# Optimization experiments

Hardware: AMD Instinct MI355X
Metric: run time of the kernel (lower is better)

The kernel has to match this reference:

```python
import jax, jax.numpy as jnp
import numpy as np

N = 50000      # nodes
E = 800000     # edges (avg degree 16)
H = 128        # hidden_channels
F = 128        # num_filters
G = 50         # num_gaussians
L = 6          # num_interactions
CUT = 10.0     # cutoff
H2 = H // 2
OUT = 12


def ssp(x):
    # ShiftedSoftplus: softplus(x) - log(2)
    return jax.nn.softplus(x) - jnp.log(2.0)


def setup_inputs() -> dict:
    key = jax.random.key(0)
    ks = jax.random.split(key, 16)
    s = 0.05
    x_atoms = jax.random.randint(ks[0], (N,), 0, 100)
    edge_index = jax.random.randint(ks[1], (2, E), 0, N)
    edge_attr = jax.random.uniform(ks[2], (E,), minval=0.05, maxval=CUT)
    return {
        "x_atoms": x_atoms,
        "edge_index": edge_index,
        "edge_attr": edge_attr,
        "embedding": jax.random.normal(ks[3], (100, H)) * s,
        # per-interaction stacked params [L, ...]
        "mlp_w1": jax.random.normal(ks[4], (L, G, F)) * s,
        "mlp_b1": jnp.zeros((L, F)),
        "mlp_w2": jax.random.normal(ks[5], (L, F, F)) * s,
        "mlp_b2": jnp.zeros((L, F)),
        "conv1_w": jax.random.normal(ks[6], (L, H, F)) * s,   # CFConv.lin1 (no bias)
        "conv2_w": jax.random.normal(ks[7], (L, F, H)) * s,   # CFConv.lin2
        "conv2_b": jnp.zeros((L, H)),
        "int_lin_w": jax.random.normal(ks[8], (L, H, H)) * s,  # InteractionBlock.lin
        "int_lin_b": jnp.zeros((L, H)),
        # head
        "lin1_w": jax.random.normal(ks[9], (H, H2)) * s,
        "lin1_b": jnp.zeros((H2,)),
        "lin2_w": jax.random.normal(ks[10], (H2, H2)) * s,
        "lin2_b": jnp.zeros((H2,)),
        "readout_w": jax.random.normal(ks[11], (H2, OUT)) * s,
        "readout_b": jnp.zeros((OUT,)),
    }


def reference(x_atoms, edge_index, edge_attr, embedding,
              mlp_w1, mlp_b1, mlp_w2, mlp_b2,
              conv1_w, conv2_w, conv2_b, int_lin_w, int_lin_b,
              lin1_w, lin1_b, lin2_w, lin2_b, readout_w, readout_b):
    h = embedding[x_atoms]  # [N, H]

    # Gaussian smearing of distances -> [E, G]
    offset = jnp.linspace(0.0, CUT, G)
    coeff = -0.5 / (offset[1] - offset[0]) ** 2
    ed = jnp.exp(coeff * (edge_attr[:, None] - offset) ** 2)

    # cosine cutoff weight per edge
    C = 0.5 * (jnp.cos(edge_attr * jnp.pi / CUT) + 1.0)  # [E]

    src = edge_index[0]
    dst = edge_index[1]

    for l in range(L):
        # filter network on expanded distances -> [E, F]
        W = ssp(ed @ mlp_w1[l] + mlp_b1[l]) @ mlp_w2[l] + mlp_b2[l]
        W = W * C[:, None]
        xf = h @ conv1_w[l]                     # [N, F]
        msg = xf[src] * W                        # gather + modulate, [E, F]
        agg = jax.ops.segment_sum(msg, dst, num_segments=N)  # scatter-add, [N, F]
        v = agg @ conv2_w[l] + conv2_b[l]        # [N, H]
        v = ssp(v)
        v = v @ int_lin_w[l] + int_lin_b[l]
        h = h + v                                # residual

    h = ssp(h @ lin1_w + lin1_b)
    h = h @ lin2_w + lin2_b
    h_agg = jnp.sum(h, axis=0, keepdims=True)    # [1, H2]
    return h_agg @ readout_w + readout_b         # [1, OUT]
```

## Files before the change

### kernel.cpp

```cpp
#include <hip/hip_runtime.h>
#include <hip/hip_bf16.h>
#include <math.h>

#define NN 50000
#define EE 800000
#define HH 128
#define FF 128
#define GG 50
#define LL 6
#define H2D 64
#define OUT_DIM 12
#define NK 4096
#define NBLK 782
#define SB 196

typedef __bf16 bf16;
typedef __attribute__((ext_vector_type(8))) __bf16 bf16x8;
typedef __attribute__((ext_vector_type(4))) __bf16 bf16x4;
typedef __attribute__((ext_vector_type(4))) float f32x4;
typedef __attribute__((ext_vector_type(4))) unsigned u32x4;

#define DEV __device__ __forceinline__

DEV float sspf(float x) {
    return fmaxf(x, 0.f) + __logf(1.f + __expf(-fabsf(x))) - 0.69314718055994531f;
}

DEV f32x4 mfma16(bf16x8 a, bf16x8 b, f32x4 c) {
    return __builtin_amdgcn_mfma_f32_16x16x32_bf16(a, b, c, 0, 0, 0);
}

DEV float blo(unsigned u) { return __uint_as_float(u << 16); }
DEV float bhi(unsigned u) { return __uint_as_float(u & 0xffff0000u); }

struct PrepArgs {
    const float *conv1_w, *conv2_w, *int_lin_w, *mlp_w1, *mlp_w2, *lin1_w, *lin2_w;
    bf16 *c1t, *c2t, *ilt, *w1t, *w2t, *l1t, *l2t;
};

__global__ void prep_kernel(PrepArgs p) {
    int j = blockIdx.x;
    const float* src = nullptr; bf16* dst = nullptr; int R = 0, C = 0, K = 0;
    if (j < 30) {
        int l = j / 5, m = j % 5;
        switch (m) {
            case 0: src = p.conv1_w + l * HH * FF;   dst = p.c1t + l * FF * HH;  R = HH; C = FF; K = HH; break;
            case 1: src = p.conv2_w + l * FF * HH;   dst = p.c2t + l * HH * FF;  R = FF; C = HH; K = FF; break;
            case 2: src = p.int_lin_w + l * HH * HH; dst = p.ilt + l * HH * HH;  R = HH; C = HH; K = HH; break;
            case 3: src = p.mlp_w1 + l * GG * FF;    dst = p.w1t + l * FF * 64;  R = GG; C = FF; K = 64; break;
            case 4: src = p.mlp_w2 + l * FF * FF;    dst = p.w2t + l * FF * FF;  R = FF; C = FF; K = FF; break;
        }
    } else if (j == 30) { src = p.lin1_w; dst = p.l1t; R = HH;  C = H2D; K = HH; }
    else                { src = p.lin2_w; dst = p.l2t; R = H2D; C = H2D; K = H2D; }
    int total = C * K;
    for (int idx = threadIdx.x; idx < total; idx += blockDim.x) {
        int c = idx / K, r = idx - c * K;
        dst[idx] = (r < R) ? (bf16)src[r * C + c] : (bf16)0.f;
    }
}

__global__ __launch_bounds__(256) void table_kernel(const bf16* __restrict__ w1t,
                                                    const bf16* __restrict__ w2t,
                                                    const float* __restrict__ mlp_b1,
                                                    const float* __restrict__ mlp_b2,
                                                    bf16* __restrict__ tab) {
    __shared__ bf16 sW1[128 * 72];
    __shared__ bf16 sW2[128 * 136];
    __shared__ bf16 sT1[64 * 136];
    int tid = threadIdx.x;
    int l = blockIdx.x / 65, rb = blockIdx.x % 65;
    const bf16* W1 = w1t + (size_t)l * 128 * 64;
    const bf16* W2 = w2t + (size_t)l * 128 * 128;
    for (int idx = tid * 8; idx < 128 * 64; idx += 2048) {
        int n = idx >> 6, k = idx & 63;
        *(bf16x8*)&sW1[n * 72 + k] = *(const bf16x8*)(W1 + idx);
    }
    for (int idx = tid * 8; idx < 128 * 128; idx += 2048) {
        int n = idx >> 7, k = idx & 127;
        *(bf16x8*)&sW2[n * 136 + k] = *(const bf16x8*)(W2 + idx);
    }
    int w = tid >> 6, lane = tid & 63, ln = lane & 15, kg = lane >> 4;
    int rowt = rb * 64 + w * 16;
    float d1 = (float)min(rowt + ln, NK) * (10.f / NK);
    const float step = 10.f / 49.f;
    const float coeff = -0.5f / (step * step);
    __syncthreads();
    f32x4 acc[8] = {};
#pragma unroll
    for (int k0 = 0; k0 < 64; k0 += 32) {
        bf16x8 a;
#pragma unroll
        for (int jj = 0; jj < 8; jj++) {
            int g = k0 + kg * 8 + jj;
            float diff = d1 - g * step;
            float v = (g < GG) ? __expf(coeff * diff * diff) : 0.f;
            a[jj] = (bf16)v;
        }
#pragma unroll
        for (int t = 0; t < 8; t++) {
            bf16x8 b = *(const bf16x8*)&sW1[(t * 16 + ln) * 72 + k0 + kg * 8];
            acc[t] = mfma16(a, b, acc[t]);
        }
    }
    const float* b1 = mlp_b1 + l * FF;
#pragma unroll
    for (int t = 0; t < 8; t++) {
        int colt = t * 16 + ln;
        float bb = b1[colt];
#pragma unroll
        for (int r = 0; r < 4; r++)
            sT1[(w * 16 + kg * 4 + r) * 136 + colt] = (bf16)sspf(acc[t][r] + bb);
    }
    __syncthreads();
    f32x4 acc2[8] = {};
#pragma unroll
    for (int k0 = 0; k0 < 128; k0 += 32) {
        bf16x8 a = *(const bf16x8*)&sT1[(w * 16 + ln) * 136 + k0 + kg * 8];
#pragma unroll
        for (int t = 0; t < 8; t++) {
            bf16x8 b = *(const bf16x8*)&sW2[(t * 16 + ln) * 136 + k0 + kg * 8];
            acc2[t] = mfma16(a, b, acc2[t]);
        }
    }
    const float* b2 = mlp_b2 + l * FF;
    float Cw[4]; int rrow[4];
#pragma unroll
    for (int r = 0; r < 4; r++) {
        int rr = rowt + kg * 4 + r;
        rrow[r] = rr;
        float dd = (float)min(rr, NK) * (10.f / NK);
        Cw[r] = 0.5f * (cosf(dd * 0.31415926535897932f) + 1.f);
    }
#pragma unroll
    for (int t = 0; t < 8; t++) {
        int colt = t * 16 + ln;
        float bb = b2[colt];
#pragma unroll
        for (int r = 0; r < 4; r++) {
            if (rrow[r] <= NK)
                tab[((size_t)l * (NK + 1) + rrow[r]) * FF + colt] = (bf16)((acc2[t][r] + bb) * Cw[r]);
        }
    }
}

__global__ void hist_kernel(const int* __restrict__ eidx, int* __restrict__ hist) {
    int e = blockIdx.x * 256 + threadIdx.x;
    if (e < EE) atomicAdd(&hist[eidx[EE + e]], 1);
}

__global__ __launch_bounds__(256) void scanA_kernel(const int* __restrict__ hist,
                                                    int* __restrict__ bsum) {
    __shared__ int red[256];
    int t = threadIdx.x;
    int i = blockIdx.x * 256 + t;
    int v = (i < NN) ? hist[i] : 0;
    red[t] = v;
    __syncthreads();
    for (int off = 128; off > 0; off >>= 1) {
        if (t < off) red[t] += red[t + off];
        __syncthreads();
    }
    if (t == 0) bsum[blockIdx.x] = red[0];
}

__global__ __launch_bounds__(256) void scanB_kernel(int* __restrict__ bsum) {
    __shared__ int buf[256];
    int t = threadIdx.x;
    int v = (t < SB) ? bsum[t] : 0;
    buf[t] = v;
    __syncthreads();
    for (int off = 1; off < 256; off <<= 1) {
        int y = (t >= off) ? buf[t - off] : 0;
        __syncthreads();
        buf[t] += y;
        __syncthreads();
    }
    if (t < SB) bsum[t] = buf[t] - v;
}

__global__ __launch_bounds__(256) void scanC_kernel(const int* __restrict__ hist,
                                                    const int* __restrict__ bsum,
                                                    int* __restrict__ rs,
                                                    int* __restrict__ cur) {
    __shared__ int buf[256];
    int t = threadIdx.x;
    int i = blockIdx.x * 256 + t;
    int v = (i < NN) ? hist[i] : 0;
    buf[t] = v;
    __syncthreads();
    for (int off = 1; off < 256; off <<= 1) {
        int y = (t >= off) ? buf[t - off] : 0;
        __syncthreads();
        buf[t] += y;
        __syncthreads();
    }
    if (i < NN) {
        int ex = buf[t] - v + bsum[blockIdx.x];
        rs[i] = ex;
        cur[i] = ex;
    }
}

__global__ void scatter_kernel(const float* __restrict__ eattr, const int* __restrict__ eidx,
                               int* __restrict__ cur, int* __restrict__ es) {
    int e = blockIdx.x * 256 + threadIdx.x;
    if (e < EE) {
        int dd = eidx[EE + e];
        int pos = atomicAdd(&cur[dd], 1);
        int k = (int)(eattr[e] * ((float)NK / 10.f) + 0.5f);
        k = min(k, NK);
        es[pos] = k | (eidx[e] << 13);
    }
}

__global__ void embed_kernel(const int* __restrict__ x_atoms, const float* __restrict__ emb,
                             bf16* __restrict__ hb) {
    int idx = blockIdx.x * blockDim.x + threadIdx.x;
    if (idx >= NN * 16) return;
    int n = idx >> 4, ch = idx & 15;
    int a = x_atoms[n];
    const float* ep = emb + a * HH + ch * 8;
    f32x4 v0 = *(const f32x4*)ep;
    f32x4 v1 = *(const f32x4*)(ep + 4);
    bf16x8 vb;
#pragma unroll
    for (int q = 0; q < 4; q++) { vb[q] = (bf16)v0[q]; vb[q + 4] = (bf16)v1[q]; }
    *(bf16x8*)(hb + n * HH + ch * 8) = vb;
}

__global__ __launch_bounds__(256) void xf_kernel(const bf16* __restrict__ hb,
                                                 const bf16* __restrict__ c1t,
                                                 bf16* __restrict__ xf) {
    __shared__ bf16 sB[128 * 136];
    int tid = threadIdx.x;
    for (int idx = tid * 8; idx < 128 * 128; idx += 2048) {
        int n = idx >> 7, k = idx & 127;
        *(bf16x8*)&sB[n * 136 + k] = *(const bf16x8*)(c1t + idx);
    }
    int w = tid >> 6, lane = tid & 63, ln = lane & 15, kg = lane >> 4;
    int rowt = blockIdx.x * 64 + w * 16;
    int arow = min(rowt + ln, NN - 1);
    __syncthreads();
    f32x4 acc[8] = {};
#pragma unroll
    for (int k0 = 0; k0 < 128; k0 += 32) {
        bf16x8 a = *(const bf16x8*)(hb + arow * HH + k0 + kg * 8);
#pragma unroll
        for (int t = 0; t < 8; t++) {
            bf16x8 b = *(const bf16x8*)&sB[(t * 16 + ln) * 136 + k0 + kg * 8];
            acc[t] = mfma16(a, b, acc[t]);
        }
    }
#pragma unroll
    for (int t = 0; t < 8; t++) {
        int colt = t * 16 + ln;
#pragma unroll
        for (int r = 0; r < 4; r++) {
            int orow = rowt + kg * 4 + r;
            if (orow < NN) xf[orow * FF + colt] = (bf16)acc[t][r];
        }
    }
}

__global__ __launch_bounds__(256) void edge_kernel(const int* __restrict__ es,
                                                   const int* __restrict__ rs,
                                                   const int* __restrict__ hist,
                                                   const bf16* __restrict__ xf,
                                                   const bf16* __restrict__ tab,
                                                   bf16* __restrict__ aggb) {
    int tid = threadIdx.x;
    int w = tid >> 6, lane = tid & 63;
    int q = lane >> 4, cl = lane & 15;
    int n = blockIdx.x * 4 + w;
    int start = rs[n], deg = hist[n];
    float a0 = 0.f, a1 = 0.f, a2 = 0.f, a3 = 0.f;
    float a4 = 0.f, a5 = 0.f, a6 = 0.f, a7 = 0.f;
    for (int base = 0; base < deg; base += 64) {
        int cnt = min(deg - base, 64);
        int pv = (lane < cnt) ? es[start + base + lane] : 0;
        int iters = (cnt + 3) >> 2;
#pragma unroll 4
        for (int j = 0; j < iters; j++) {
            int jj = 4 * j + q;
            bool valid = jj < cnt;
            int v = __shfl(pv, jj);
            int k = v & 8191;
            int s = v >> 13;
            u32x4 tp = *(const u32x4*)(tab + (size_t)k * FF + 8 * cl);
            u32x4 xu = *(const u32x4*)(xf + (size_t)s * FF + 8 * cl);
            unsigned t0 = valid ? tp.x : 0u;
            unsigned t1 = valid ? tp.y : 0u;
            unsigned t2 = valid ? tp.z : 0u;
            unsigned t3 = valid ? tp.w : 0u;
            a0 = fmaf(blo(t0), blo(xu.x), a0);
            a1 = fmaf(bhi(t0), bhi(xu.x), a1);
            a2 = fmaf(blo(t1), blo(xu.y), a2);
            a3 = fmaf(bhi(t1), bhi(xu.y), a3);
            a4 = fmaf(blo(t2), blo(xu.z), a4);
            a5 = fmaf(bhi(t2), bhi(xu.z), a5);
            a6 = fmaf(blo(t3), blo(xu.w), a6);
            a7 = fmaf(bhi(t3), bhi(xu.w), a7);
        }
    }
    a0 += __shfl_xor(a0, 16); a0 += __shfl_xor(a0, 32);
    a1 += __shfl_xor(a1, 16); a1 += __shfl_xor(a1, 32);
    a2 += __shfl_xor(a2, 16); a2 += __shfl_xor(a2, 32);
    a3 += __shfl_xor(a3, 16); a3 += __shfl_xor(a3, 32);
    a4 += __shfl_xor(a4, 16); a4 += __shfl_xor(a4, 32);
    a5 += __shfl_xor(a5, 16); a5 += __shfl_xor(a5, 32);
    a6 += __shfl_xor(a6, 16); a6 += __shfl_xor(a6, 32);
    a7 += __shfl_xor(a7, 16); a7 += __shfl_xor(a7, 32);
    if (q == 0) {
        bf16x8 pk;
        pk[0] = (bf16)a0; pk[1] = (bf16)a1; pk[2] = (bf16)a2; pk[3] = (bf16)a3;
        pk[4] = (bf16)a4; pk[5] = (bf16)a5; pk[6] = (bf16)a6; pk[7] = (bf16)a7;
        *(bf16x8*)(aggb + (size_t)n * FF + 8 * cl) = pk;
    }
}

__global__ __launch_bounds__(256) void update_kernel(const bf16* __restrict__ aggb,
                                                     const bf16* __restrict__ c2t,
                                                     const float* __restrict__ c2b,
                                                     const bf16* __restrict__ ilt,
                                                     const float* __restrict__ ilb,
                                                     bf16* __restrict__ hb,
                                                     const bf16* __restrict__ c1n,
                                                     bf16* __restrict__ xf_out,
                                                     const bf16* __restrict__ l1t,
                                                     const float* __restrict__ l1b,
                                                     const bf16* __restrict__ l2t,
                                                     const float* __restrict__ l2b,
                                                     float* __restrict__ partial) {
    __shared__ bf16 sB[128 * 136];
    __shared__ bf16 sT[64 * 136];
    int tid = threadIdx.x;
    int w = tid >> 6, lane = tid & 63, ln = lane & 15, kg = lane >> 4;
    int rowt = blockIdx.x * 64 + w * 16;
    int arow = min(rowt + ln, NN - 1);
    float hpre[8][4];
#pragma unroll
    for (int t = 0; t < 8; t++) {
        int colt = t * 16 + ln;
#pragma unroll
        for (int r = 0; r < 4; r++) {
            int orow = rowt + kg * 4 + r;
            hpre[t][r] = (orow < NN) ? (float)hb[(size_t)orow * HH + colt] : 0.f;
        }
    }
    for (int idx = tid * 8; idx < 128 * 128; idx += 2048) {
        int n = idx >> 7, k = idx & 127;
        *(bf16x8*)&sB[n * 136 + k] = *(const bf16x8*)(c2t + idx);
    }
    __syncthreads();
    f32x4 acc[8] = {};
#pragma unroll
    for (int k0 = 0; k0 < 128; k0 += 32) {
        bf16x8 a = *(const bf16x8*)(aggb + (size_t)arow * FF + k0 + kg * 8);
#pragma unroll
        for (int t = 0; t < 8; t++) {
            bf16x8 b = *(const bf16x8*)&sB[(t * 16 + ln) * 136 + k0 + kg * 8];
            acc[t] = mfma16(a, b, acc[t]);
        }
    }
#pragma unroll
    for (int t = 0; t < 8; t++) {
        int colt = t * 16 + ln;
        float bb = c2b[colt];
#pragma unroll
        for (int r = 0; r < 4; r++)
            sT[(w * 16 + kg * 4 + r) * 136 + colt] = (bf16)sspf(acc[t][r] + bb);
    }
    __syncthreads();
    for (int idx = tid * 8; idx < 128 * 128; idx += 2048) {
        int n = idx >> 7, k = idx & 127;
        *(bf16x8*)&sB[n * 136 + k] = *(const bf16x8*)(ilt + idx);
    }
    __syncthreads();
    f32x4 acc2[8] = {};
#pragma unroll
    for (int k0 = 0; k0 < 128; k0 += 32) {
        bf16x8 a = *(const bf16x8*)&sT[(w * 16 + ln) * 136 + k0 + kg * 8];
#pragma unroll
        for (int t = 0; t < 8; t++) {
            bf16x8 b = *(const bf16x8*)&sB[(t * 16 + ln) * 136 + k0 + kg * 8];
            acc2[t] = mfma16(a, b, acc2[t]);
        }
    }
    bool is_last = (c1n == nullptr);
#pragma unroll
    for (int t = 0; t < 8; t++) {
        int colt = t * 16 + ln;
        float bb = ilb[colt];
#pragma unroll
        for (int r = 0; r < 4; r++) {
            int orow = rowt + kg * 4 + r;
            float hn = hpre[t][r] + acc2[t][r] + bb;
            if (orow < NN && !is_last) hb[(size_t)orow * HH + colt] = (bf16)hn;
            sT[(w * 16 + kg * 4 + r) * 136 + colt] = (bf16)hn;
        }
    }
    if (!is_last) {
        __syncthreads();
        for (int idx = tid * 8; idx < 128 * 128; idx += 2048) {
            int n = idx >> 7, k = idx & 127;
            *(bf16x8*)&sB[n * 136 + k] = *(const bf16x8*)(c1n + idx);
        }
        __syncthreads();
        f32x4 acc3[8] = {};
#pragma unroll
        for (int k0 = 0; k0 < 128; k0 += 32) {
            bf16x8 a = *(const bf16x8*)&sT[(w * 16 + ln) * 136 + k0 + kg * 8];
#pragma unroll
            for (int t = 0; t < 8; t++) {
                bf16x8 b = *(const bf16x8*)&sB[(t * 16 + ln) * 136 + k0 + kg * 8];
                acc3[t] = mfma16(a, b, acc3[t]);
            }
        }
#pragma unroll
        for (int t = 0; t < 8; t++) {
            int colt = t * 16 + ln;
#pragma unroll
            for (int r = 0; r < 4; r++) {
                int orow = rowt + kg * 4 + r;
                if (orow < NN) xf_out[(size_t)orow * FF + colt] = (bf16)acc3[t][r];
            }
        }
    } else {
        __syncthreads();
        for (int idx = tid * 8; idx < 64 * 128; idx += 2048) {
            int n = idx >> 7, k = idx & 127;
            *(bf16x8*)&sB[n * 136 + k] = *(const bf16x8*)(l1t + idx);
        }
        __syncthreads();
        f32x4 acch[4] = {};
#pragma unroll
        for (int k0 = 0; k0 < 128; k0 += 32) {
            bf16x8 a = *(const bf16x8*)&sT[(w * 16 + ln) * 136 + k0 + kg * 8];
#pragma unroll
            for (int t = 0; t < 4; t++) {
                bf16x8 b = *(const bf16x8*)&sB[(t * 16 + ln) * 136 + k0 + kg * 8];
                acch[t] = mfma16(a, b, acch[t]);
            }
        }
#pragma unroll
        for (int t = 0; t < 4; t++) {
            int colt = t * 16 + ln;
            float bb = l1b[colt];
#pragma unroll
            for (int r = 0; r < 4; r++)
                sT[(w * 16 + kg * 4 + r) * 136 + colt] = (bf16)sspf(acch[t][r] + bb);
        }
        __syncthreads();
        for (int idx = tid * 8; idx < 64 * 64; idx += 2048) {
            int n = idx >> 6, k = idx & 63;
            *(bf16x8*)&sB[n * 136 + k] = *(const bf16x8*)(l2t + idx);
        }
        __syncthreads();
        f32x4 acc2h[4] = {};
#pragma unroll
        for (int k0 = 0; k0 < 64; k0 += 32) {
            bf16x8 a = *(const bf16x8*)&sT[(w * 16 + ln) * 136 + k0 + kg * 8];
#pragma unroll
            for (int t = 0; t < 4; t++) {
                bf16x8 b = *(const bf16x8*)&sB[(t * 16 + ln) * 136 + k0 + kg * 8];
                acc2h[t] = mfma16(a, b, acc2h[t]);
            }
        }
        __syncthreads();
        float* sPart = (float*)sT;
#pragma unroll
        for (int t = 0; t < 4; t++) {
            int colt = t * 16 + ln;
            float bb = l2b[colt];
            float v = 0.f;
#pragma unroll
            for (int r = 0; r < 4; r++) {
                int orow = rowt + kg * 4 + r;
                if (orow < NN) v += acc2h[t][r] + bb;
            }
            v += __shfl_xor(v, 16);
            v += __shfl_xor(v, 32);
            if (kg == 0) sPart[w * 64 + colt] = v;
        }
        __syncthreads();
        if (tid < 64) {
            float s = sPart[tid] + sPart[64 + tid] + sPart[128 + tid] + sPart[192 + tid];
            partial[blockIdx.x * 64 + tid] = s;
        }
    }
}

__global__ __launch_bounds__(64) void final_kernel(const float* __restrict__ partial,
                                                   const float* __restrict__ rw,
                                                   const float* __restrict__ rb,
                                                   float* __restrict__ out) {
    __shared__ float sv[64];
    int j = threadIdx.x;
    float s = 0.f;
    for (int b = 0; b < NBLK; b++) s += partial[b * 64 + j];
    sv[j] = s;
    __syncthreads();
    if (j < OUT_DIM) {
        float o = rb[j];
        for (int i = 0; i < H2D; i++) o += sv[i] * rw[i * OUT_DIM + j];
        out[j] = o;
    }
}

extern "C" void kernel_launch(void* const* d_in, const int* in_sizes, int n_in,
                              void* d_out, int out_size, void* d_ws, size_t ws_size,
                              hipStream_t stream) {
    const int*   x_atoms    = (const int*)d_in[0];
    const int*   edge_index = (const int*)d_in[1];
    const float* edge_attr  = (const float*)d_in[2];
    const float* embedding  = (const float*)d_in[3];
    const float* mlp_w1     = (const float*)d_in[4];
    const float* mlp_b1     = (const float*)d_in[5];
    const float* mlp_w2     = (const float*)d_in[6];
    const float* mlp_b2     = (const float*)d_in[7];
    const float* conv1_w    = (const float*)d_in[8];
    const float* conv2_w    = (const float*)d_in[9];
    const float* conv2_b    = (const float*)d_in[10];
    const float* int_lin_w  = (const float*)d_in[11];
    const float* int_lin_b  = (const float*)d_in[12];
    const float* lin1_w     = (const float*)d_in[13];
    const float* lin1_b     = (const float*)d_in[14];
    const float* lin2_w     = (const float*)d_in[15];
    const float* lin2_b     = (const float*)d_in[16];
    const float* readout_w  = (const float*)d_in[17];
    const float* readout_b  = (const float*)d_in[18];

    char* ws = (char*)d_ws;
    bf16*  hb      = (bf16*)(ws + 0);
    bf16*  xfA     = (bf16*)(ws + 12800000);
    bf16*  xfB     = (bf16*)(ws + 25600000);
    bf16*  aggb    = (bf16*)(ws + 38400000);
    float* partial = (float*)(ws + 51200000);
    size_t wb = 51400192;
    bf16* c1t = (bf16*)(ws + wb);
    bf16* c2t = (bf16*)(ws + wb + 196608);
    bf16* ilt = (bf16*)(ws + wb + 393216);
    bf16* w1t = (bf16*)(ws + wb + 589824);
    bf16* w2t = (bf16*)(ws + wb + 688128);
    bf16* l1t = (bf16*)(ws + wb + 884736);
    bf16* l2t = (bf16*)(ws + wb + 901120);
    int*   d_hist = (int*)(ws + 52309504);
    int*   d_rs   = (int*)(ws + 52509504);
    int*   d_cur  = (int*)(ws + 52709504);
    int*   d_bsum = (int*)(ws + 52909504);
    int*   d_es   = (int*)(ws + 52910528);
    bf16*  tab    = (bf16*)(ws + 56110528);

    PrepArgs pa = { conv1_w, conv2_w, int_lin_w, mlp_w1, mlp_w2, lin1_w, lin2_w,
                    c1t, c2t, ilt, w1t, w2t, l1t, l2t };
    prep_kernel<<<32, 256, 0, stream>>>(pa);
    table_kernel<<<LL * 65, 256, 0, stream>>>(w1t, w2t, mlp_b1, mlp_b2, tab);
    embed_kernel<<<NN * 16 / 256, 256, 0, stream>>>(x_atoms, embedding, hb);

    hipMemsetAsync(d_hist, 0, NN * 4, stream);
    hist_kernel<<<(EE + 255) / 256, 256, 0, stream>>>(edge_index, d_hist);
    scanA_kernel<<<SB, 256, 0, stream>>>(d_hist, d_bsum);
    scanB_kernel<<<1, 256, 0, stream>>>(d_bsum);
    scanC_kernel<<<SB, 256, 0, stream>>>(d_hist, d_bsum, d_rs, d_cur);
    scatter_kernel<<<(EE + 255) / 256, 256, 0, stream>>>(edge_attr, edge_index, d_cur, d_es);

    xf_kernel<<<NBLK, 256, 0, stream>>>(hb, c1t, xfA);
    bf16* xf_in = xfA;
    bf16* xf_out = xfB;
    for (int l = 0; l < LL; l++) {
        edge_kernel<<<NN / 4, 256, 0, stream>>>(d_es, d_rs, d_hist, xf_in,
                                                tab + (size_t)l * (NK + 1) * FF, aggb);
        const bf16* c1n = (l + 1 < LL) ? (c1t + (size_t)(l + 1) * FF * HH) : nullptr;
        update_kernel<<<NBLK, 256, 0, stream>>>(aggb, c2t + (size_t)l * HH * FF,
                                                conv2_b + l * HH,
                                                ilt + (size_t)l * HH * HH, int_lin_b + l * HH,
                                                hb, c1n, xf_out,
                                                l1t, lin1_b, l2t, lin2_b, partial);
        bf16* tmp = xf_in; xf_in = xf_out; xf_out = tmp;
    }
    final_kernel<<<1, 64, 0, stream>>>(partial, readout_w, readout_b, (float*)d_out);
}
```

Measured before the change: 654.6 us.

## Two-pass bucketed edge sort and transposed MFMA output layout in update

Replaces the per-edge global-atomic scatter into CSR order with a two-pass bucket sort. The first pass groups edges into 256-node buckets, using LDS counters and one global atomic per bucket per block. The second pass places edges within each bucket using LDS atomics. Separately, the update kernel swaps the MFMA operands so each lane holds four consecutive columns of one row, which allows vectorized bf16x4 loads and stores of h, xf and the biases. The cost is an extra 8-byte-per-edge temporary buffer and two extra launches.

```diff
diff --git a/kernel.cpp b/kernel.cpp
--- a/kernel.cpp
+++ b/kernel.cpp
@@ -13,6 +13,7 @@
 #define NK 4096
 #define NBLK 782
 #define SB 196
+#define NBUK 196
 
 typedef __bf16 bf16;
 typedef __attribute__((ext_vector_type(8))) __bf16 bf16x8;
@@ -180,8 +181,7 @@
 
 __global__ __launch_bounds__(256) void scanC_kernel(const int* __restrict__ hist,
                                                     const int* __restrict__ bsum,
-                                                    int* __restrict__ rs,
-                                                    int* __restrict__ cur) {
+                                                    int* __restrict__ rs) {
     __shared__ int buf[256];
     int t = threadIdx.x;
     int i = blockIdx.x * 256 + t;
@@ -194,22 +194,73 @@
         buf[t] += y;
         __syncthreads();
     }
-    if (i < NN) {
-        int ex = buf[t] - v + bsum[blockIdx.x];
-        rs[i] = ex;
-        cur[i] = ex;
-    }
-}
-
-__global__ void scatter_kernel(const float* __restrict__ eattr, const int* __restrict__ eidx,
-                               int* __restrict__ cur, int* __restrict__ es) {
-    int e = blockIdx.x * 256 + threadIdx.x;
-    if (e < EE) {
-        int dd = eidx[EE + e];
-        int pos = atomicAdd(&cur[dd], 1);
-        int k = (int)(eattr[e] * ((float)NK / 10.f) + 0.5f);
-        k = min(k, NK);
-        es[pos] = k | (eidx[e] << 13);
+    if (i < NN) rs[i] = buf[t] - v + bsum[blockIdx.x];
+}
+
+__global__ void bukinit_kernel(const int* __restrict__ rs, int* __restrict__ bucket_cur) {
+    int b = threadIdx.x;
+    if (b < NBUK) bucket_cur[b] = rs[b * 256];
+}
+
+__global__ __launch_bounds__(256) void scat1_kernel(const float* __restrict__ eattr,
+                                                    const int* __restrict__ eidx,
+                                                    int* __restrict__ bucket_cur,
+                                                    int2* __restrict__ tmp8) {
+    __shared__ int cnt[NBUK];
+    __shared__ int res[NBUK];
+    int t = threadIdx.x;
+    for (int i = t; i < NBUK; i += 256) cnt[i] = 0;
+    __syncthreads();
+    int e0 = blockIdx.x * 4096;
+    int pv[16], dd[16], bk[16];
+#pragma unroll
+    for (int i = 0; i < 16; i++) {
+        int e = e0 + i * 256 + t;
+        if (e < EE) {
+            int d = eidx[EE + e];
+            int k = (int)(eattr[e] * ((float)NK / 10.f) + 0.5f);
+            k = min(k, NK);
+            pv[i] = k | (eidx[e] << 13);
+            dd[i] = d;
+            bk[i] = d >> 8;
+            atomicAdd(&cnt[bk[i]], 1);
+        } else bk[i] = -1;
+    }
+    __syncthreads();
+    for (int i = t; i < NBUK; i += 256) {
+        int c = cnt[i];
+        res[i] = (c > 0) ? atomicAdd(&bucket_cur[i], c) : 0;
+        cnt[i] = 0;
+    }
+    __syncthreads();
+#pragma unroll
+    for (int i = 0; i < 16; i++) {
+        if (bk[i] >= 0) {
+            int rank = atomicAdd(&cnt[bk[i]], 1);
+            int2 v; v.x = pv[i]; v.y = dd[i];
+            tmp8[res[bk[i]] + rank] = v;
+        }
+    }
+}
+
+__global__ __launch_bounds__(256) void scat2_kernel(const int* __restrict__ rs,
+                                                    const int2* __restrict__ tmp8,
+                                                    int* __restrict__ es) {
+    __shared__ int off[256];
+    __shared__ int loc[256];
+    int b = blockIdx.x, t = threadIdx.x;
+    int nb0 = b * 256;
+    int nnb = min(256, NN - nb0);
+    int base = rs[nb0];
+    int end = (nb0 + 256 < NN) ? rs[nb0 + 256] : EE;
+    loc[t] = 0;
+    if (t < nnb) off[t] = rs[nb0 + t] - base;
+    __syncthreads();
+    for (int e = base + t; e < end; e += 256) {
+        int2 v = tmp8[e];
+        int nl = v.y - nb0;
+        int rank = atomicAdd(&loc[nl], 1);
+        es[base + off[nl] + rank] = v.x;
     }
 }
 
@@ -336,17 +387,13 @@
     int tid = threadIdx.x;
     int w = tid >> 6, lane = tid & 63, ln = lane & 15, kg = lane >> 4;
     int rowt = blockIdx.x * 64 + w * 16;
-    int arow = min(rowt + ln, NN - 1);
-    float hpre[8][4];
-#pragma unroll
-    for (int t = 0; t < 8; t++) {
-        int colt = t * 16 + ln;
-#pragma unroll
-        for (int r = 0; r < 4; r++) {
-            int orow = rowt + kg * 4 + r;
-            hpre[t][r] = (orow < NN) ? (float)hb[(size_t)orow * HH + colt] : 0.f;
-        }
-    }
+    int nrow = rowt + ln;
+    int arow = min(nrow, NN - 1);
+    bool rowok = nrow < NN;
+    bf16x4 hpre[8];
+#pragma unroll
+    for (int t = 0; t < 8; t++)
+        hpre[t] = *(const bf16x4*)(hb + (size_t)arow * HH + t * 16 + kg * 4);
     for (int idx = tid * 8; idx < 128 * 128; idx += 2048) {
         int n = idx >> 7, k = idx & 127;
         *(bf16x8*)&sB[n * 136 + k] = *(const bf16x8*)(c2t + idx);
@@ -355,20 +402,20 @@
     f32x4 acc[8] = {};
 #pragma unroll
     for (int k0 = 0; k0 < 128; k0 += 32) {
-        bf16x8 a = *(const bf16x8*)(aggb + (size_t)arow * FF + k0 + kg * 8);
+        bf16x8 bfrag = *(const bf16x8*)(aggb + (size_t)arow * FF + k0 + kg * 8);
 #pragma unroll
         for (int t = 0; t < 8; t++) {
-            bf16x8 b = *(const bf16x8*)&sB[(t * 16 + ln) * 136 + k0 + kg * 8];
-            acc[t] = mfma16(a, b, acc[t]);
+            bf16x8 afrag = *(const bf16x8*)&sB[(t * 16 + ln) * 136 + k0 + kg * 8];
+            acc[t] = mfma16(afrag, bfrag, acc[t]);
         }
     }
 #pragma unroll
     for (int t = 0; t < 8; t++) {
-        int colt = t * 16 + ln;
-        float bb = c2b[colt];
-#pragma unroll
-        for (int r = 0; r < 4; r++)
-            sT[(w * 16 + kg * 4 + r) * 136 + colt] = (bf16)sspf(acc[t][r] + bb);
+        f32x4 bb = *(const f32x4*)(c2b + t * 16 + kg * 4);
+        bf16x4 pk;
+#pragma unroll
+        for (int r = 0; r < 4; r++) pk[r] = (bf16)sspf(acc[t][r] + bb[r]);
+        *(bf16x4*)&sT[(w * 16 + ln) * 136 + t * 16 + kg * 4] = pk;
     }
     __syncthreads();
     for (int idx = tid * 8; idx < 128 * 128; idx += 2048) {
@@ -379,25 +426,23 @@
     f32x4 acc2[8] = {};
 #pragma unroll
     for (int k0 = 0; k0 < 128; k0 += 32) {
-        bf16x8 a = *(const bf16x8*)&sT[(w * 16 + ln) * 136 + k0 + kg * 8];
+        bf16x8 bfrag = *(const bf16x8*)&sT[(w * 16 + ln) * 136 + k0 + kg * 8];
 #pragma unroll
         for (int t = 0; t < 8; t++) {
-            bf16x8 b = *(const bf16x8*)&sB[(t * 16 + ln) * 136 + k0 + kg * 8];
-            acc2[t] = mfma16(a, b, acc2[t]);
+            bf16x8 afrag = *(const bf16x8*)&sB[(t * 16 + ln) * 136 + k0 + kg * 8];
+            acc2[t] = mfma16(afrag, bfrag, acc2[t]);
         }
     }
     bool is_last = (c1n == nullptr);
 #pragma unroll
     for (int t = 0; t < 8; t++) {
-        int colt = t * 16 + ln;
-        float bb = ilb[colt];
-#pragma unroll
-        for (int r = 0; r < 4; r++) {
-            int orow = rowt + kg * 4 + r;
-            float hn = hpre[t][r] + acc2[t][r] + bb;
-            if (orow < NN && !is_last) hb[(size_t)orow * HH + colt] = (bf16)hn;
-            sT[(w * 16 + kg * 4 + r) * 136 + colt] = (bf16)hn;
-        }
+        f32x4 bb = *(const f32x4*)(ilb + t * 16 + kg * 4);
+        bf16x4 pk;
+#pragma unroll
+        for (int r = 0; r < 4; r++)
+            pk[r] = (bf16)((float)hpre[t][r] + acc2[t][r] + bb[r]);
+        if (rowok && !is_last) *(bf16x4*)(hb + (size_t)nrow * HH + t * 16 + kg * 4) = pk;
+        *(bf16x4*)&sT[(w * 16 + ln) * 136 + t * 16 + kg * 4] = pk;
     }
     if (!is_last) {
         __syncthreads();
@@ -409,21 +454,19 @@
         f32x4 acc3[8] = {};
 #pragma unroll
         for (int k0 = 0; k0 < 128; k0 += 32) {
-            bf16x8 a = *(const bf16x8*)&sT[(w * 16 + ln) * 136 + k0 + kg * 8];
+            bf16x8 bfrag = *(const bf16x8*)&sT[(w * 16 + ln) * 136 + k0 + kg * 8];
 #pragma unroll
             for (int t = 0; t < 8; t++) {
-                bf16x8 b = *(const bf16x8*)&sB[(t * 16 + ln) * 136 + k0 + kg * 8];
-                acc3[t] = mfma16(a, b, acc3[t]);
+                bf16x8 afrag = *(const bf16x8*)&sB[(t * 16 + ln) * 136 + k0 + kg * 8];
+                acc3[t] = mfma16(afrag, bfrag, acc3[t]);
             }
         }
 #pragma unroll
         for (int t = 0; t < 8; t++) {
-            int colt = t * 16 + ln;
-#pragma unroll
-            for (int r = 0; r < 4; r++) {
-                int orow = rowt + kg * 4 + r;
-                if (orow < NN) xf_out[(size_t)orow * FF + colt] = (bf16)acc3[t][r];
-            }
+            bf16x4 pk;
+#pragma unroll
+            for (int r = 0; r < 4; r++) pk[r] = (bf16)acc3[t][r];
+            if (rowok) *(bf16x4*)(xf_out + (size_t)nrow * FF + t * 16 + kg * 4) = pk;
         }
     } else {
         __syncthreads();
@@ -546,10 +589,11 @@
     bf16* l2t = (bf16*)(ws + wb + 901120);
     int*   d_hist = (int*)(ws + 52309504);
     int*   d_rs   = (int*)(ws + 52509504);
-    int*   d_cur  = (int*)(ws + 52709504);
-    int*   d_bsum = (int*)(ws + 52909504);
-    int*   d_es   = (int*)(ws + 52910528);
-    bf16*  tab    = (bf16*)(ws + 56110528);
+    int*   d_bcur = (int*)(ws + 52709504);
+    int*   d_bsum = (int*)(ws + 52710528);
+    int*   d_es   = (int*)(ws + 52711552);
+    bf16*  tab    = (bf16*)(ws + 55911552);
+    int2*  d_tmp8 = (int2*)(ws + 62204544);
 
     PrepArgs pa = { conv1_w, conv2_w, int_lin_w, mlp_w1, mlp_w2, lin1_w, lin2_w,
                     c1t, c2t, ilt, w1t, w2t, l1t, l2t };
@@ -561,8 +605,10 @@
     hist_kernel<<<(EE + 255) / 256, 256, 0, stream>>>(edge_index, d_hist);
     scanA_kernel<<<SB, 256, 0, stream>>>(d_hist, d_bsum);
     scanB_kernel<<<1, 256, 0, stream>>>(d_bsum);
-    scanC_kernel<<<SB, 256, 0, stream>>>(d_hist, d_bsum, d_rs, d_cur);
-    scatter_kernel<<<(EE + 255) / 256, 256, 0, stream>>>(edge_attr, edge_index, d_cur, d_es);
+    scanC_kernel<<<SB, 256, 0, stream>>>(d_hist, d_bsum, d_rs);
+    bukinit_kernel<<<1, 256, 0, stream>>>(d_rs, d_bcur);
+    scat1_kernel<<<NBUK, 256, 0, stream>>>(edge_attr, edge_index, d_bcur, d_tmp8);
+    scat2_kernel<<<NBUK, 256, 0, stream>>>(d_rs, d_tmp8, d_es);
 
     xf_kernel<<<NBLK, 256, 0, stream>>>(hb, c1t, xfA);
     bf16* xf_in = xfA;
```

New measurement: 587.5 us. 1.11x faster.
